# Kernel optimization log

Hardware: AMD Instinct MI355X
Metric: run time of the kernel (lower is better)

## Reference

```python
import jax, jax.numpy as jnp
import numpy as np
import math

C_IN = 256
NUM_CLASSES = 80
NUM_CONVS = 3
GROUPS = 16
EPS = 1e-5
FEAT_SHAPES = [(2, C_IN, 100, 128), (2, C_IN, 50, 64), (2, C_IN, 25, 32), (2, C_IN, 13, 16), (2, C_IN, 7, 8)]


def conv2d(x, w, b):
    # x: [N,C,H,W], w: [O,I,3,3] -> SAME padding, stride 1
    y = jax.lax.conv_general_dilated(x, w, window_strides=(1, 1), padding='SAME',
                                     dimension_numbers=('NCHW', 'OIHW', 'NCHW'))
    return y + b[None, :, None, None]


def group_norm(x, gamma, beta):
    N, C, H, W = x.shape
    xr = x.reshape(N, GROUPS, C // GROUPS, H, W)
    m = xr.mean(axis=(2, 3, 4), keepdims=True)
    v = xr.var(axis=(2, 3, 4), keepdims=True)
    xn = ((xr - m) * jax.lax.rsqrt(v + EPS)).reshape(N, C, H, W)
    return xn * gamma[None, :, None, None] + beta[None, :, None, None]


def tower(x, ws, bs, gs, gbs):
    for i in range(NUM_CONVS):
        x = jax.nn.relu(group_norm(conv2d(x, ws[i], bs[i]), gs[i], gbs[i]))
    return x


def permut(x):
    # torch permutTensor: [N,C,H,W] -> [N, H*W, C]
    N, C, H, W = x.shape
    return x.transpose(0, 2, 3, 1).reshape(N, H * W, C)


def setup_inputs() -> dict:
    key = jax.random.key(0)
    ks = list(jax.random.split(key, 32))
    d = {}
    for i, shp in enumerate(FEAT_SHAPES):
        d[f'feat{i + 3}'] = jax.random.normal(ks[i], shp, dtype=jnp.float32)
    std = 0.01
    d['cls_conv_w'] = jax.random.normal(ks[5], (NUM_CONVS, C_IN, C_IN, 3, 3), dtype=jnp.float32) * std
    d['cls_conv_b'] = jnp.zeros((NUM_CONVS, C_IN), jnp.float32)
    d['cls_gn_g'] = jnp.ones((NUM_CONVS, C_IN), jnp.float32)
    d['cls_gn_b'] = jnp.zeros((NUM_CONVS, C_IN), jnp.float32)
    d['cls_logits_w'] = jax.random.normal(ks[6], (NUM_CLASSES, C_IN, 3, 3), dtype=jnp.float32) * std
    d['cls_logits_b'] = jnp.full((NUM_CLASSES,), -math.log((1 - 0.01) / 0.01), jnp.float32)
    d['reg_conv_w'] = jax.random.normal(ks[7], (NUM_CONVS, C_IN, C_IN, 3, 3), dtype=jnp.float32) * std
    d['reg_conv_b'] = jnp.zeros((NUM_CONVS, C_IN), jnp.float32)
    d['reg_gn_g'] = jnp.ones((NUM_CONVS, C_IN), jnp.float32)
    d['reg_gn_b'] = jnp.zeros((NUM_CONVS, C_IN), jnp.float32)
    d['bbox_reg_w'] = jax.random.normal(ks[8], (4, C_IN, 3, 3), dtype=jnp.float32) * std
    d['bbox_reg_b'] = jnp.zeros((4,), jnp.float32)
    d['ctr_w'] = jax.random.normal(ks[9], (1, C_IN, 3, 3), dtype=jnp.float32) * std
    d['ctr_b'] = jnp.zeros((1,), jnp.float32)
    return d


def reference(feat3, feat4, feat5, feat6, feat7,
              cls_conv_w, cls_conv_b, cls_gn_g, cls_gn_b, cls_logits_w, cls_logits_b,
              reg_conv_w, reg_conv_b, reg_gn_g, reg_gn_b,
              bbox_reg_w, bbox_reg_b, ctr_w, ctr_b):
    feats = [feat3, feat4, feat5, feat6, feat7]
    per_level = []
    for f in feats:
        # classification branch
        c = tower(f, cls_conv_w, cls_conv_b, cls_gn_g, cls_gn_b)
        cls = permut(conv2d(c, cls_logits_w, cls_logits_b))          # [N, HW, 80]
        r = tower(f, reg_conv_w, reg_conv_b, reg_gn_g, reg_gn_b)
        reg = permut(jax.nn.relu(conv2d(r, bbox_reg_w, bbox_reg_b)))  # [N, HW, 4]
        ctr = permut(conv2d(r, ctr_w, ctr_b))                         # [N, HW, 1]
        per_level.append(jnp.concatenate([cls, reg, ctr], axis=-1))
    # concat over pyramid levels -> [N, total_points, 85]
    return jnp.concatenate(per_level, axis=1)
```

## Files before the change

kernel.cpp:

```cpp
#include <hip/hip_runtime.h>

#define NCLS 80
#define TPOINTS 17064
#define GN_EPS 1e-5f

typedef float v4f __attribute__((ext_vector_type(4)));
typedef short v8s __attribute__((ext_vector_type(8)));

__device__ __forceinline__ unsigned short f2bf(float f) {
    unsigned u = __float_as_uint(f);
    unsigned r = (u + 0x7FFFu + ((u >> 16) & 1u)) >> 16;
    return (unsigned short)r;
}
__device__ __forceinline__ float bf2f(unsigned short h) {
    return __uint_as_float(((unsigned)h) << 16);
}
__device__ __forceinline__ void gload16(const unsigned short* g, unsigned short* l) {
    __builtin_amdgcn_global_load_lds(
        (const __attribute__((address_space(1))) unsigned int*)g,
        (__attribute__((address_space(3))) unsigned int*)l, 16, 0, 0);
}
template<int N> __device__ __forceinline__ void vwait() {
    asm volatile("s_waitcnt vmcnt(%0)" :: "n"(N) : "memory");
    __builtin_amdgcn_sched_barrier(0);
}
#define LGKM0 do { asm volatile("s_waitcnt lgkmcnt(0)" ::: "memory"); \
                   __builtin_amdgcn_sched_barrier(0); } while (0)

struct Lv { int t_conv, t_gn, t_prep, t_h5, xo, P2W, PP, HW, W, H, lwW, loff; };
struct Tab { Lv lv[5]; };

template<int HEAD>
__global__ __launch_bounds__(512, 4) void conv_k(
    const unsigned short* __restrict__ xin, size_t xin_brs,
    const unsigned short* __restrict__ wt, size_t wt_brs, int wrows,
    const float* __restrict__ bias_c, const float* __restrict__ bias_r,
    unsigned short* __restrict__ yout, float* __restrict__ stats, int layer,
    float* __restrict__ out,
    Tab tb)
{
    __shared__ __align__(16) unsigned short sA[3 * 256 * 32];
    __shared__ __align__(16) unsigned short sB[3 * 128 * 32];
    const int tid = threadIdx.x, lane = tid & 63, wave = tid >> 6;
    const int bx = blockIdx.x, z = blockIdx.z;
    const int n = z & 1, br = z >> 1;
    int L = 0;
    while (L < 4 && bx >= tb.lv[L + 1].t_conv) ++L;
    const Lv lv = tb.lv[L];
    const int pp0 = (bx - lv.t_conv) * 128;
    const size_t XELs = 9200640;
    const size_t PP32 = (size_t)lv.PP * 32;

    v4f acc[4][4];
#pragma unroll
    for (int i = 0; i < 4; ++i)
#pragma unroll
        for (int j = 0; j < 4; ++j) acc[i][j] = (v4f)0.f;

    const unsigned short* wtb = wt + (size_t)br * wt_brs;
    const float* bias = br ? bias_r : bias_c;
    const unsigned short* xb = xin + (size_t)br * xin_brs +
                               (size_t)lv.xo + (size_t)n * lv.PP * 256;

    const int lr = lane >> 2;
    const int lc = ((lane & 3) ^ ((lane >> 3) & 3)) * 8;
    const unsigned short* ag = wtb + (size_t)(wave * 32 + lr) * 32 + lc;
    const unsigned short* bgh = xb + (ptrdiff_t)(pp0 + wave * 16 + lr) * 32 + lc;
    unsigned short* laW = &sA[wave * 32 * 32];
    unsigned short* lbW = &sB[wave * 16 * 32];
    const size_t wstride2 = (size_t)wrows * 32;

    const int col = lane & 15, q = lane >> 4;
    const int wr = wave & 3, wc = wave >> 2;
    const int qs = (q ^ ((col >> 1) & 3)) << 3;
    int ard[4], brd[4];
#pragma unroll
    for (int i = 0; i < 4; ++i) ard[i] = (wr * 64 + i * 16 + col) * 32 + qs;
#pragma unroll
    for (int j = 0; j < 4; ++j) brd[j] = (wc * 64 + j * 16 + col) * 32 + qs;

    auto stageHalf = [&](int s) {
        const int slot = s % 3;
        const unsigned short* at = ag + (size_t)s * wstride2;
        gload16(at,       laW + slot * 8192);
        gload16(at + 512, laW + slot * 8192 + 512);
        const int t = s >> 3, kb = s & 7;
        const ptrdiff_t goff = ((ptrdiff_t)(t / 3) - 1) * lv.P2W + (t % 3) - 1;
        gload16(bgh + (size_t)kb * PP32 + goff * 32, lbW + slot * 4096);
    };

    auto half_body = [&](int h, bool dostage) {
        const int sa = (h % 3) * 8192, sb_ = (h % 3) * 4096;
        v8s af[4], bfr[4];
#pragma unroll
        for (int i = 0; i < 4; ++i) af[i]  = *(const v8s*)&sA[sa + ard[i]];
#pragma unroll
        for (int j = 0; j < 4; ++j) bfr[j] = *(const v8s*)&sB[sb_ + brd[j]];
        LGKM0;
        __builtin_amdgcn_s_barrier();
        if (dostage) stageHalf(h + 3);
        __builtin_amdgcn_sched_barrier(0);
        __builtin_amdgcn_s_setprio(1);
#pragma unroll
        for (int i = 0; i < 4; ++i)
#pragma unroll
            for (int j = 0; j < 4; ++j)
                acc[i][j] = __builtin_amdgcn_mfma_f32_16x16x32_bf16(
                    af[i], bfr[j], acc[i][j], 0, 0, 0);
        __builtin_amdgcn_s_setprio(0);
    };

    stageHalf(0); stageHalf(1); stageHalf(2);
#pragma unroll 1
    for (int h = 0; h < 70; ++h) {
        vwait<6>();
        __builtin_amdgcn_s_barrier();
        half_body(h, h < 69);
    }
    vwait<3>(); __builtin_amdgcn_s_barrier(); half_body(70, false);
    vwait<0>(); __builtin_amdgcn_s_barrier(); half_body(71, false);

    if (!HEAD) {
        unsigned short* yb = yout + (size_t)br * XELs + (size_t)lv.xo +
                             (size_t)n * lv.PP * 256;
        const int slot = br * 3 + layer;
#pragma unroll
        for (int i = 0; i < 4; ++i) {
            const int cobase = wr * 64 + i * 16 + q * 4;
            const float4 b4 = *(const float4*)(bias + cobase);
            const size_t kbo = (size_t)(cobase >> 5) * PP32;
            const int cc = cobase & 31;
            float s = 0.f, ss = 0.f;
#pragma unroll
            for (int j = 0; j < 4; ++j) {
                const int pp = pp0 + wc * 64 + j * 16 + col;
                const unsigned h2 = (unsigned)pp / (unsigned)lv.P2W;
                const unsigned w2 = (unsigned)pp - h2 * lv.P2W;
                const bool in = (h2 >= 1u) & (h2 <= (unsigned)lv.H) &
                                (w2 >= 1u) & (w2 <= (unsigned)lv.W);
                float v0 = acc[i][j][0] + b4.x;
                float v1 = acc[i][j][1] + b4.y;
                float v2 = acc[i][j][2] + b4.z;
                float v3 = acc[i][j][3] + b4.w;
                if (in) {
                    ushort4 pk;
                    pk.x = f2bf(v0); pk.y = f2bf(v1);
                    pk.z = f2bf(v2); pk.w = f2bf(v3);
                    *(ushort4*)(yb + kbo + (size_t)pp * 32 + cc) = pk;
                    s  += v0 + v1 + v2 + v3;
                    ss += v0 * v0 + v1 * v1 + v2 * v2 + v3 * v3;
                }
            }
#pragma unroll
            for (int o = 32; o > 0; o >>= 1) {
                s  += __shfl_down(s, o, 64);
                ss += __shfl_down(ss, o, 64);
            }
            if (lane == 0) {
                const int g = cobase >> 4;
                const int si = (((slot * 5 + L) * 32) + n * 16 + g) * 2;
                atomicAdd(&stats[si + 0], s);
                atomicAdd(&stats[si + 1], ss);
            }
        }
    } else {
        const int CO_ = br ? 5 : 80;
        const int coo = br ? 80 : 0;
        const int rel = br ? 4 : 0;
#pragma unroll
        for (int i = 0; i < 4; ++i) {
            const int cobase = wr * 64 + i * 16 + q * 4;
            float bv[4];
#pragma unroll
            for (int k = 0; k < 4; ++k)
                bv[k] = (cobase + k < CO_) ? bias[cobase + k] : 0.f;
#pragma unroll
            for (int j = 0; j < 4; ++j) {
                const int pp = pp0 + wc * 64 + j * 16 + col;
                const unsigned h2 = (unsigned)pp / (unsigned)lv.P2W;
                const unsigned w2 = (unsigned)pp - h2 * lv.P2W;
                const bool in = (h2 >= 1u) & (h2 <= (unsigned)lv.H) &
                                (w2 >= 1u) & (w2 <= (unsigned)lv.W);
                if (in) {
                    const int p = (h2 - 1) * lv.W + (w2 - 1);
                    float* ob = out + ((size_t)n * TPOINTS + lv.loff + p) * 85 + coo;
#pragma unroll
                    for (int k = 0; k < 4; ++k) {
                        const int co = cobase + k;
                        if (co < CO_) {
                            float v = acc[i][j][k] + bv[k];
                            if (co < rel) v = fmaxf(v, 0.f);
                            ob[co] = v;
                        }
                    }
                }
            }
        }
    }
}

__global__ __launch_bounds__(256) void gn_k(
    unsigned short* __restrict__ x, const float* __restrict__ stats, int layer,
    const float* __restrict__ g_c, const float* __restrict__ be_c,
    const float* __restrict__ g_r, const float* __restrict__ be_r, Tab tb)
{
    const int tid = threadIdx.x, bx = blockIdx.x, z = blockIdx.z;
    const int n = z & 1, br = z >> 1;
    const size_t XELs = 9200640;
    int L = 0;
    while (L < 4 && bx >= tb.lv[L + 1].t_gn) ++L;
    const Lv lv = tb.lv[L];
    const int pos = (bx - lv.t_gn) * 32 + (tid >> 3);
    if (pos >= lv.HW) return;
    const int slot = br * 3 + layer;
    const float* gamma = (br ? g_r : g_c) + layer * 256;
    const float* beta  = (br ? be_r : be_c) + layer * 256;
    const int c0 = (tid & 7) * 32;
    const int h = pos >> lv.lwW, w = pos & (lv.W - 1);
    const int pp = (h + 1) * lv.P2W + (w + 1);
    unsigned short* p = x + (size_t)br * XELs + (size_t)lv.xo +
                        (size_t)n * lv.PP * 256 +
                        (size_t)(tid & 7) * lv.PP * 32 + (size_t)pp * 32;
    const float inv = 1.0f / (16.0f * (float)lv.HW);
    const int sb = ((slot * 5 + L) * 32 + n * 16) * 2;

    float scv[32], shv[32];
#pragma unroll
    for (int gg = 0; gg < 2; ++gg) {
        const int g = (c0 >> 4) + gg;
        const float mm = stats[sb + g * 2 + 0] * inv;
        const float v = stats[sb + g * 2 + 1] * inv - mm * mm;
        const float rs = rsqrtf(v + GN_EPS);
#pragma unroll
        for (int k = 0; k < 16; ++k) {
            const int c = g * 16 + k;
            const float sc = rs * gamma[c];
            scv[gg * 16 + k] = sc;
            shv[gg * 16 + k] = beta[c] - mm * sc;
        }
    }
#pragma unroll
    for (int u = 0; u < 4; ++u) {
        uint4 a = *(const uint4*)(p + u * 8);
        unsigned wds[4] = {a.x, a.y, a.z, a.w};
#pragma unroll
        for (int k = 0; k < 4; ++k) {
            const int e = u * 8 + k * 2;
            float lo = bf2f((unsigned short)(wds[k] & 0xffffu));
            float hi = bf2f((unsigned short)(wds[k] >> 16));
            lo = fmaxf(lo * scv[e]     + shv[e],     0.f);
            hi = fmaxf(hi * scv[e + 1] + shv[e + 1], 0.f);
            wds[k] = (unsigned)f2bf(lo) | ((unsigned)f2bf(hi) << 16);
        }
        uint4 o; o.x = wds[0]; o.y = wds[1]; o.z = wds[2]; o.w = wds[3];
        *(uint4*)(p + u * 8) = o;
    }
}

__global__ __launch_bounds__(256) void prepx_k(
    const float* f0, const float* f1, const float* f2, const float* f3,
    const float* f4, unsigned short* __restrict__ xo, Tab tb)
{
    const float* fs[5] = {f0, f1, f2, f3, f4};
    const int tid = threadIdx.x, bx = blockIdx.x, n = blockIdx.z;
    int L = 0;
    while (L < 4 && bx >= tb.lv[L + 1].t_prep) ++L;
    const Lv lv = tb.lv[L];
    const int pos = (bx - lv.t_prep) * 64 + (tid & 63);
    const int wave = tid >> 6;
    if (pos >= lv.HW) return;
    const int h = pos >> lv.lwW, w = pos & (lv.W - 1);
    const int pp = (h + 1) * lv.P2W + (w + 1);
    const float* src = fs[L] + (size_t)n * 256 * lv.HW + pos;
    unsigned short* dst = xo + (size_t)lv.xo + (size_t)n * lv.PP * 256;
#pragma unroll
    for (int k = 0; k < 16; ++k) {
        const int c = wave * 64 + k * 4;
        ushort4 pk;
        pk.x = f2bf(src[(size_t)(c + 0) * lv.HW]);
        pk.y = f2bf(src[(size_t)(c + 1) * lv.HW]);
        pk.z = f2bf(src[(size_t)(c + 2) * lv.HW]);
        pk.w = f2bf(src[(size_t)(c + 3) * lv.HW]);
        *(ushort4*)(dst + (size_t)(c >> 5) * lv.PP * 32 +
                    (size_t)pp * 32 + (c & 31)) = pk;
    }
}

__global__ __launch_bounds__(256) void prepwt_k(
    const float* __restrict__ cw, const float* __restrict__ rw,
    unsigned short* __restrict__ dst)
{
    const int idx = blockIdx.x * 256 + threadIdx.x;
    const int ci = idx & 255, co = (idx >> 8) & 255, r = idx >> 16;
    const int tap = r % 9, layer = (r / 9) % 3, br = r / 27;
    const float* s = br ? rw : cw;
    dst[(size_t)r * 65536 + (size_t)(((ci >> 5) * 256 + co) * 32) + (ci & 31)] =
        f2bf(s[(((size_t)layer * 256 + co) * 256 + ci) * 9 + tap]);
}

__global__ __launch_bounds__(256) void prepwh_k(
    const float* __restrict__ src, unsigned short* __restrict__ dst,
    int CO, int rows, int roff)
{
    const int idx = blockIdx.x * 256 + threadIdx.x;
    if (idx >= CO * 2304) return;
    const int ci = idx & 255, rr = idx >> 8;
    const int tap = rr % 9, co = rr / 9;
    dst[((size_t)(tap * 8 + (ci >> 5)) * rows + roff + co) * 32 + (ci & 31)] =
        f2bf(src[((size_t)co * 256 + ci) * 9 + tap]);
}

extern "C" void kernel_launch(void* const* d_in, const int* in_sizes, int n_in,
                              void* d_out, int out_size, void* d_ws, size_t ws_size,
                              hipStream_t stream) {
    const float* f0 = (const float*)d_in[0];
    const float* f1 = (const float*)d_in[1];
    const float* f2 = (const float*)d_in[2];
    const float* f3 = (const float*)d_in[3];
    const float* f4 = (const float*)d_in[4];
    const float* cls_w  = (const float*)d_in[5];
    const float* cls_b  = (const float*)d_in[6];
    const float* cls_g  = (const float*)d_in[7];
    const float* cls_be = (const float*)d_in[8];
    const float* log_w  = (const float*)d_in[9];
    const float* log_b  = (const float*)d_in[10];
    const float* reg_w  = (const float*)d_in[11];
    const float* reg_b  = (const float*)d_in[12];
    const float* reg_g  = (const float*)d_in[13];
    const float* reg_be = (const float*)d_in[14];
    const float* bbox_w = (const float*)d_in[15];
    const float* bbox_b = (const float*)d_in[16];
    const float* ctr_w  = (const float*)d_in[17];
    const float* ctr_b  = (const float*)d_in[18];
    float* out = (float*)d_out;

    Tab tb;
    tb.lv[0] = {   0,    0,    0,    0,   0,       130, 13260, 12800, 128, 100, 7, 0     };
    tb.lv[1] = { 104,  400,  200,  52,  6789120,    66,  3432,  3200,  64,  50, 6, 12800 };
    tb.lv[2] = { 131,  500,  250,  66,  8546304,    34,   918,   800,  32,  25, 5, 16000 };
    tb.lv[3] = { 139,  525,  263,  70,  9016320,    18,   270,   208,  16,  13, 4, 16800 };
    tb.lv[4] = { 142,  532,  267,  72,  9154560,    10,    90,    56,   8,   7, 3, 17008 };
    const int NT_CONV = 143, NT_GN = 534, NT_PREP = 268;
    const size_t XEL = 9200640;
    const size_t WHP = (size_t)72 * 256 * 32;

    char* base = (char*)d_ws;
    size_t o = 0;
    auto take = [&](size_t bytes) {
        char* p = base + o; o += (bytes + 255) & ~(size_t)255; return p;
    };
    take(131072);
    unsigned short* PX = (unsigned short*)take(XEL * 2);
    take(131072);
    unsigned short* B1 = (unsigned short*)take(XEL * 2 * 2);
    take(131072);
    unsigned short* B2 = (unsigned short*)take(XEL * 2 * 2);
    take(131072);
    unsigned short* WT = (unsigned short*)take((size_t)54 * 65536 * 2);
    unsigned short* WH = (unsigned short*)take(WHP * 2 * 2);
    float* ST  = (float*)take(1920 * 4);
    float* RB5 = (float*)take(32);

    hipMemsetAsync(PX, 0, XEL * 2, stream);
    hipMemsetAsync(B1, 0, XEL * 4, stream);
    hipMemsetAsync(B2, 0, XEL * 4, stream);
    hipMemsetAsync(ST, 0, 1920 * 4, stream);
    hipMemsetAsync(WH, 0, WHP * 2 * 2, stream);
    hipMemcpyAsync(RB5,     bbox_b, 4 * 4, hipMemcpyDeviceToDevice, stream);
    hipMemcpyAsync(RB5 + 4, ctr_b,  1 * 4, hipMemcpyDeviceToDevice, stream);

    prepwt_k<<<dim3(13824), dim3(256), 0, stream>>>(cls_w, reg_w, WT);
    prepwh_k<<<dim3(720), dim3(256), 0, stream>>>(log_w,  WH,       80, 256, 0);
    prepwh_k<<<dim3(36),  dim3(256), 0, stream>>>(bbox_w, WH + WHP,  4, 256, 0);
    prepwh_k<<<dim3(9),   dim3(256), 0, stream>>>(ctr_w,  WH + WHP,  1, 256, 4);

    prepx_k<<<dim3(NT_PREP, 1, 2), dim3(256), 0, stream>>>(f0, f1, f2, f3, f4, PX, tb);

    const size_t WBRS = (size_t)27 * 65536;
    unsigned short* cin[3]  = {PX, B1, B2};
    size_t          cbrs[3] = {0, XEL, XEL};
    unsigned short* cout_[3] = {B1, B2, B1};
    for (int i = 0; i < 3; ++i) {
        conv_k<0><<<dim3(NT_CONV, 1, 4), dim3(512), 0, stream>>>(
            cin[i], cbrs[i], WT + (size_t)i * 9 * 65536, WBRS, 256,
            cls_b + i * 256, reg_b + i * 256,
            cout_[i], ST, i, nullptr, tb);
        gn_k<<<dim3(NT_GN, 1, 4), dim3(256), 0, stream>>>(
            cout_[i], ST, i, cls_g, cls_be, reg_g, reg_be, tb);
    }
    conv_k<1><<<dim3(NT_CONV, 1, 4), dim3(512), 0, stream>>>(
        B1, XEL, WH, WHP, 256, log_b, RB5,
        nullptr, nullptr, 0, out, tb);
}
```

Before: 917.1 us.

## Load conv weight fragments directly from global into registers, drop LDS staging for A

Weight (A) fragments are no longer staged into shared memory with global_load_lds. Each wave now reads its four bf16 fragments straight from global memory into registers on every half-step. The activation (B) ring buffer grows from 3 to 4 slots, and the vmcnt waits and barrier placement are reworked. This aims to cut LDS traffic and footprint and drop the lgkm wait, but it exposes global/L2 latency for A on every step, with only 16 MFMAs available to hide it, and duplicates weight reads across waves.

```diff
diff --git a/kernel.cpp b/kernel.cpp
--- a/kernel.cpp
+++ b/kernel.cpp
@@ -24,8 +24,6 @@
     asm volatile("s_waitcnt vmcnt(%0)" :: "n"(N) : "memory");
     __builtin_amdgcn_sched_barrier(0);
 }
-#define LGKM0 do { asm volatile("s_waitcnt lgkmcnt(0)" ::: "memory"); \
-                   __builtin_amdgcn_sched_barrier(0); } while (0)
 
 struct Lv { int t_conv, t_gn, t_prep, t_h5, xo, P2W, PP, HW, W, H, lwW, loff; };
 struct Tab { Lv lv[5]; };
@@ -39,8 +37,7 @@
     float* __restrict__ out,
     Tab tb)
 {
-    __shared__ __align__(16) unsigned short sA[3 * 256 * 32];
-    __shared__ __align__(16) unsigned short sB[3 * 128 * 32];
+    __shared__ __align__(16) unsigned short sB[4 * 128 * 32];
     const int tid = threadIdx.x, lane = tid & 63, wave = tid >> 6;
     const int bx = blockIdx.x, z = blockIdx.z;
     const int n = z & 1, br = z >> 1;
@@ -64,42 +61,43 @@
 
     const int lr = lane >> 2;
     const int lc = ((lane & 3) ^ ((lane >> 3) & 3)) * 8;
-    const unsigned short* ag = wtb + (size_t)(wave * 32 + lr) * 32 + lc;
     const unsigned short* bgh = xb + (ptrdiff_t)(pp0 + wave * 16 + lr) * 32 + lc;
-    unsigned short* laW = &sA[wave * 32 * 32];
     unsigned short* lbW = &sB[wave * 16 * 32];
     const size_t wstride2 = (size_t)wrows * 32;
 
     const int col = lane & 15, q = lane >> 4;
     const int wr = wave & 3, wc = wave >> 2;
     const int qs = (q ^ ((col >> 1) & 3)) << 3;
-    int ard[4], brd[4];
-#pragma unroll
-    for (int i = 0; i < 4; ++i) ard[i] = (wr * 64 + i * 16 + col) * 32 + qs;
+    int brd[4];
 #pragma unroll
     for (int j = 0; j < 4; ++j) brd[j] = (wc * 64 + j * 16 + col) * 32 + qs;
 
-    auto stageHalf = [&](int s) {
-        const int slot = s % 3;
-        const unsigned short* at = ag + (size_t)s * wstride2;
-        gload16(at,       laW + slot * 8192);
-        gload16(at + 512, laW + slot * 8192 + 512);
+    const unsigned short* agf = wtb + (size_t)(wr * 64 + col) * 32 + q * 8;
+
+    auto stageB = [&](int s) {
         const int t = s >> 3, kb = s & 7;
         const ptrdiff_t goff = ((ptrdiff_t)(t / 3) - 1) * lv.P2W + (t % 3) - 1;
-        gload16(bgh + (size_t)kb * PP32 + goff * 32, lbW + slot * 4096);
+        gload16(bgh + (size_t)kb * PP32 + goff * 32,
+                lbW + (s & 3) * 4096);
     };
 
-    auto half_body = [&](int h, bool dostage) {
-        const int sa = (h % 3) * 8192, sb_ = (h % 3) * 4096;
-        v8s af[4], bfr[4];
-#pragma unroll
-        for (int i = 0; i < 4; ++i) af[i]  = *(const v8s*)&sA[sa + ard[i]];
+    auto half_body = [&](int h, int dostage) {
+        const unsigned short* at = agf + (size_t)h * wstride2;
+        v8s af[4];
+#pragma unroll
+        for (int i = 0; i < 4; ++i)
+            af[i] = *(const v8s*)(at + i * 512);
+        if (h < 69)      vwait<6>();
+        else if (h == 69) vwait<6>();
+        else if (h == 70) vwait<5>();
+        else              vwait<4>();
+        __builtin_amdgcn_s_barrier();
+        __builtin_amdgcn_sched_barrier(0);
+        if (dostage) stageB(h + 3);
+        const int sb_ = (h & 3) * 4096;
+        v8s bfr[4];
 #pragma unroll
         for (int j = 0; j < 4; ++j) bfr[j] = *(const v8s*)&sB[sb_ + brd[j]];
-        LGKM0;
-        __builtin_amdgcn_s_barrier();
-        if (dostage) stageHalf(h + 3);
-        __builtin_amdgcn_sched_barrier(0);
         __builtin_amdgcn_s_setprio(1);
 #pragma unroll
         for (int i = 0; i < 4; ++i)
@@ -110,15 +108,12 @@
         __builtin_amdgcn_s_setprio(0);
     };
 
-    stageHalf(0); stageHalf(1); stageHalf(2);
+    stageB(0); stageB(1); stageB(2);
 #pragma unroll 1
-    for (int h = 0; h < 70; ++h) {
-        vwait<6>();
-        __builtin_amdgcn_s_barrier();
-        half_body(h, h < 69);
-    }
-    vwait<3>(); __builtin_amdgcn_s_barrier(); half_body(70, false);
-    vwait<0>(); __builtin_amdgcn_s_barrier(); half_body(71, false);
+    for (int h = 0; h < 69; ++h) half_body(h, 1);
+    half_body(69, 0);
+    half_body(70, 0);
+    half_body(71, 0);
 
     if (!HEAD) {
         unsigned short* yb = yout + (size_t)br * XELs + (size_t)lv.xo +
```

Result: slower. 1.071 ms (+16.8%).
